# Kernel tuning notes

Hardware: AMD Instinct MI355X
Metric: run time of the kernel (lower is better)

Reference implementation:

```python
import jax, jax.numpy as jnp
import numpy as np

HEADS = 4
LOCAL_CTX = 8  # local_attn_ctx (stride)


def _strided_transpose(x, n_ctx, local_ctx):
    # [B, n_ctx, E] -> reshape [B, n_ctx//local, local, E] -> swap -> [B, n_ctx, E]
    B, _, E = x.shape
    bT = n_ctx // local_ctx
    return x.reshape(B, bT, local_ctx, E).transpose(0, 2, 1, 3).reshape(B, n_ctx, E)


def _strided_untranspose(a, n_ctx, local_ctx):
    B, _, E = a.shape
    bT = n_ctx // local_ctx
    return a.reshape(B, local_ctx, bT, E).transpose(0, 2, 1, 3).reshape(B, n_ctx, E)


def setup_inputs() -> dict:
    key = jax.random.key(0)
    ks = jax.random.split(key, 6)
    B, T, E = 2048, 64, 256
    value = jax.random.normal(ks[0], (B, T, E), dtype=jnp.float32)
    k_in = jax.random.normal(ks[1], (B, T, E), dtype=jnp.float32)
    query = jax.random.normal(ks[2], (B, T, E), dtype=jnp.float32)
    mask = jnp.ones((B, T), dtype=jnp.int32)  # unused by the block
    W_ff = jax.random.normal(ks[3], (256, T * E), dtype=jnp.float32) * (1.0 / np.sqrt(T * E))
    b_ff = jax.random.normal(ks[4], (256,), dtype=jnp.float32) * 0.01
    return {"value": value, "key": k_in, "query": query, "mask": mask, "W_ff": W_ff, "b_ff": b_ff}


def reference(value, key, query, mask, W_ff, b_ff):
    B, n_ctx, E = query.shape
    # strided transpose of q, k, v
    q = _strided_transpose(query, n_ctx, LOCAL_CTX)
    k = _strided_transpose(key, n_ctx, LOCAL_CTX)
    v = _strided_transpose(value, n_ctx, LOCAL_CTX)
    scale = 1.0 / np.sqrt(E // HEADS)  # n_state = embd // heads
    w = jax.nn.softmax(jnp.einsum('bqe,bke->bqk', q, k) * scale, axis=-1)
    a = jnp.einsum('bqk,bke->bqe', w, v)
    attention = _strided_untranspose(a, n_ctx, LOCAL_CTX)
    # residual + dropout (eval-mode identity)
    x = attention + query
    # flatten-linear + ReLU
    out = jax.nn.relu(x.reshape(B, n_ctx * E) @ W_ff.T + b_ff)
    return (out, attention)
```

## Files before the change

### kernel.cpp

```cpp
#include <hip/hip_runtime.h>
#include <stdint.h>

typedef __attribute__((ext_vector_type(8))) short s16x8;
typedef __attribute__((ext_vector_type(4))) float f32x4;

__device__ __forceinline__ unsigned short f2bf(float f) {
  unsigned int u = __float_as_uint(f);
  u += 0x7fffu + ((u >> 16) & 1u);
  return (unsigned short)(u >> 16);
}
__device__ __forceinline__ float bf2f(unsigned short h) {
  return __uint_as_float(((unsigned int)h) << 16);
}
__device__ __forceinline__ f32x4 mfma16(s16x8 a, s16x8 b, f32x4 c) {
  return __builtin_amdgcn_mfma_f32_16x16x32_bf16(a, b, c, 0, 0, 0);
}

#define KH_STR 136
#define VT_STR 72
#define P_STR  72

__global__ __launch_bounds__(256) void attn_kernel(
    const float* __restrict__ Vg, const float* __restrict__ Kg,
    const float* __restrict__ Qg, float* __restrict__ attn_out,
    unsigned short* __restrict__ xb ) {
  __shared__ __align__(16) char smem[46080];
  unsigned short* KhL = (unsigned short*)smem;
  unsigned short* KlL = (unsigned short*)(smem + 17408);
  unsigned short* VtL = (unsigned short*)smem;
  unsigned short* PL  = (unsigned short*)(smem + 36864);

  const int b = blockIdx.x;
  const int tid = threadIdx.x;
  const int lane = tid & 63;
  const int w = tid >> 6;
  const int n = lane & 15;
  const int q = lane >> 4;

  const float* Qb = Qg + (size_t)b * 64 * 256;
  const float* Kb = Kg + (size_t)b * 64 * 256;
  const float* Vb = Vg + (size_t)b * 64 * 256;

  f32x4 accS[4];
#pragma unroll
  for (int c = 0; c < 4; ++c) accS[c] = f32x4{0.f, 0.f, 0.f, 0.f};

  for (int ph = 0; ph < 2; ++ph) {
    const int e0 = ph * 128;
#pragma unroll
    for (int it = 0; it < 8; ++it) {
      int i = it * 256 + tid;
      int row = i >> 5;
      int c4 = i & 31;
      float4 v = *(const float4*)(Kb + row * 256 + e0 + c4 * 4);
      ushort4 hi, lo;
      hi.x = f2bf(v.x); lo.x = f2bf(v.x - bf2f(hi.x));
      hi.y = f2bf(v.y); lo.y = f2bf(v.y - bf2f(hi.y));
      hi.z = f2bf(v.z); lo.z = f2bf(v.z - bf2f(hi.z));
      hi.w = f2bf(v.w); lo.w = f2bf(v.w - bf2f(hi.w));
      *(ushort4*)(KhL + row * KH_STR + c4 * 4) = hi;
      *(ushort4*)(KlL + row * KH_STR + c4 * 4) = lo;
    }
    __syncthreads();
#pragma unroll
    for (int kk = 0; kk < 4; ++kk) {
      const float* qsrc = Qb + (16 * w + n) * 256 + e0 + kk * 32 + q * 8;
      float4 a0 = *(const float4*)qsrc;
      float4 a1 = *(const float4*)(qsrc + 4);
      float av[8] = {a0.x, a0.y, a0.z, a0.w, a1.x, a1.y, a1.z, a1.w};
      s16x8 qh, ql;
#pragma unroll
      for (int j = 0; j < 8; ++j) {
        unsigned short h = f2bf(av[j]);
        qh[j] = (short)h;
        ql[j] = (short)f2bf(av[j] - bf2f(h));
      }
      const int colb = kk * 32 + q * 8;
#pragma unroll
      for (int c = 0; c < 4; ++c) {
        s16x8 kh = *(const s16x8*)(KhL + (16 * c + n) * KH_STR + colb);
        s16x8 kl = *(const s16x8*)(KlL + (16 * c + n) * KH_STR + colb);
        accS[c] = mfma16(qh, kh, accS[c]);
        accS[c] = mfma16(qh, kl, accS[c]);
        accS[c] = mfma16(ql, kh, accS[c]);
      }
    }
    __syncthreads();
  }

  const float scale = 0.125f;
  float p[4][4];
#pragma unroll
  for (int r = 0; r < 4; ++r) {
    float m = -1e30f;
#pragma unroll
    for (int c = 0; c < 4; ++c) m = fmaxf(m, accS[c][r]);
#pragma unroll
    for (int mk = 1; mk < 16; mk <<= 1) m = fmaxf(m, __shfl_xor(m, mk, 64));
    float s = 0.f;
#pragma unroll
    for (int c = 0; c < 4; ++c) {
      float e = __expf((accS[c][r] - m) * scale);
      p[c][r] = e;
      s += e;
    }
#pragma unroll
    for (int mk = 1; mk < 16; mk <<= 1) s += __shfl_xor(s, mk, 64);
    float inv = 1.0f / s;
#pragma unroll
    for (int c = 0; c < 4; ++c) p[c][r] *= inv;
  }

#pragma unroll 4
  for (int t2 = 0; t2 < 32; ++t2) {
    int t = t2 * 2;
    float v0 = Vb[t * 256 + tid];
    float v1 = Vb[(t + 1) * 256 + tid];
    unsigned int pk = (unsigned int)f2bf(v0) | ((unsigned int)f2bf(v1) << 16);
    *(unsigned int*)(VtL + tid * VT_STR + t) = pk;
  }
#pragma unroll
  for (int r = 0; r < 4; ++r) {
    int row = 16 * w + 4 * q + r;
#pragma unroll
    for (int c = 0; c < 4; ++c) PL[row * P_STR + 16 * c + n] = f2bf(p[c][r]);
  }
  __syncthreads();

  f32x4 accA[16];
#pragma unroll
  for (int c = 0; c < 16; ++c) accA[c] = f32x4{0.f, 0.f, 0.f, 0.f};
#pragma unroll
  for (int ks = 0; ks < 2; ++ks) {
    const int colb = ks * 32 + q * 8;
    s16x8 af = *(const s16x8*)(PL + (16 * w + n) * P_STR + colb);
#pragma unroll
    for (int c = 0; c < 16; ++c) {
      s16x8 bf = *(const s16x8*)(VtL + (16 * c + n) * VT_STR + colb);
      accA[c] = mfma16(af, bf, accA[c]);
    }
  }

#pragma unroll
  for (int r = 0; r < 4; ++r) {
    int t = 16 * w + 4 * q + r;
    size_t base = ((size_t)b * 64 + t) * 256;
#pragma unroll
    for (int c = 0; c < 16; ++c) {
      int e = 16 * c + n;
      float aval = accA[c][r];
      attn_out[base + e] = aval;
      if (xb) xb[base + e] = f2bf(aval + Qb[t * 256 + e]);
    }
  }
}

__global__ __launch_bounds__(256) void w2b_kernel(const float* __restrict__ W,
                                                  unsigned short* __restrict__ Wb) {
  int i = blockIdx.x * 256 + threadIdx.x;
  float4 v = ((const float4*)W)[i];
  ushort4 o;
  o.x = f2bf(v.x); o.y = f2bf(v.y); o.z = f2bf(v.z); o.w = f2bf(v.w);
  ((ushort4*)Wb)[i] = o;
}

template <bool USE_XB>
__global__ __launch_bounds__(256) void ff_kernel(
    const unsigned short* __restrict__ xb, const float* __restrict__ attn,
    const float* __restrict__ query, const unsigned short* __restrict__ Wb,
    float* __restrict__ part, int kchunk) {
  __shared__ __align__(16) unsigned short As[64 * 72];
  __shared__ __align__(16) unsigned short Bs[64 * 72];
  const int tid = threadIdx.x;
  const int lane = tid & 63, w = tid >> 6, n = lane & 15, q = lane >> 4;
  const int m0 = blockIdx.x * 64;
  const int n0 = blockIdx.y * 64;
  const int k0 = blockIdx.z * kchunk;

  f32x4 acc[4];
#pragma unroll
  for (int c = 0; c < 4; ++c) acc[c] = f32x4{0.f, 0.f, 0.f, 0.f};

  const int srow = tid >> 3;
  const int scol = (tid & 7) * 8;

  for (int kk = 0; kk < kchunk; kk += 64) {
#pragma unroll
    for (int rr = 0; rr < 2; ++rr) {
      int row = rr * 32 + srow;
      size_t ga = (size_t)(m0 + row) * 16384 + k0 + kk + scol;
      if (USE_XB) {
        *(uint4*)(As + row * 72 + scol) = *(const uint4*)(xb + ga);
      } else {
        float4 a0 = *(const float4*)(attn + ga);
        float4 a1 = *(const float4*)(attn + ga + 4);
        float4 q0 = *(const float4*)(query + ga);
        float4 q1 = *(const float4*)(query + ga + 4);
        ushort4 h0, h1;
        h0.x = f2bf(a0.x + q0.x); h0.y = f2bf(a0.y + q0.y);
        h0.z = f2bf(a0.z + q0.z); h0.w = f2bf(a0.w + q0.w);
        h1.x = f2bf(a1.x + q1.x); h1.y = f2bf(a1.y + q1.y);
        h1.z = f2bf(a1.z + q1.z); h1.w = f2bf(a1.w + q1.w);
        *(ushort4*)(As + row * 72 + scol) = h0;
        *(ushort4*)(As + row * 72 + scol + 4) = h1;
      }
      size_t gw = (size_t)(n0 + row) * 16384 + k0 + kk + scol;
      *(uint4*)(Bs + row * 72 + scol) = *(const uint4*)(Wb + gw);
    }
    __syncthreads();
#pragma unroll
    for (int ks = 0; ks < 2; ++ks) {
      const int colb = ks * 32 + q * 8;
      s16x8 af = *(const s16x8*)(As + (16 * w + n) * 72 + colb);
#pragma unroll
      for (int c = 0; c < 4; ++c) {
        s16x8 bf = *(const s16x8*)(Bs + (16 * c + n) * 72 + colb);
        acc[c] = mfma16(af, bf, acc[c]);
      }
    }
    __syncthreads();
  }
#pragma unroll
  for (int r = 0; r < 4; ++r) {
    int m = m0 + 16 * w + 4 * q + r;
#pragma unroll
    for (int c = 0; c < 4; ++c) {
      int nn = n0 + 16 * c + n;
      part[((size_t)blockIdx.z * 2048 + m) * 256 + nn] = acc[c][r];
    }
  }
}

__global__ __launch_bounds__(256) void relu_kernel(const float* __restrict__ part,
                                                   const float* __restrict__ bias,
                                                   float* __restrict__ out, int KS) {
  int idx = blockIdx.x * 256 + threadIdx.x;
  float s = bias[idx & 255];
  for (int ks = 0; ks < KS; ++ks) s += part[(size_t)ks * 2048 * 256 + idx];
  out[idx] = fmaxf(s, 0.f);
}

extern "C" void kernel_launch(void* const* d_in, const int* in_sizes, int n_in,
                              void* d_out, int out_size, void* d_ws, size_t ws_size,
                              hipStream_t stream) {
  const float* value = (const float*)d_in[0];
  const float* key   = (const float*)d_in[1];
  const float* query = (const float*)d_in[2];
  const float* W_ff  = (const float*)d_in[4];
  const float* b_ff  = (const float*)d_in[5];

  float* out  = (float*)d_out;
  float* attn = out + (size_t)2048 * 256;

  const int KS = 4;
  const size_t wb_bytes   = (size_t)256 * 16384 * 2;
  const size_t part_bytes = (size_t)KS * 2048 * 256 * 4;
  const size_t xb_bytes   = (size_t)2048 * 64 * 256 * 2;
  unsigned short* Wb = (unsigned short*)d_ws;
  float* part = (float*)((char*)d_ws + wb_bytes);
  bool use_xb = ws_size >= wb_bytes + part_bytes + xb_bytes;
  unsigned short* xb =
      use_xb ? (unsigned short*)((char*)d_ws + wb_bytes + part_bytes) : nullptr;

  w2b_kernel<<<4096, 256, 0, stream>>>(W_ff, Wb);
  attn_kernel<<<2048, 256, 0, stream>>>(value, key, query, attn, xb);
  dim3 gb(32, 4, KS);
  if (use_xb)
    ff_kernel<true><<<gb, 256, 0, stream>>>(xb, nullptr, nullptr, Wb, part, 16384 / KS);
  else
    ff_kernel<false><<<gb, 256, 0, stream>>>(nullptr, attn, query, Wb, part, 16384 / KS);
  relu_kernel<<<2048, 256, 0, stream>>>(part, b_ff, out, KS);
}
```

Measured before the change: 287.4 us.

## Shrink LDS, prefetch V into registers, swizzle K tiles, stage coalesced output

```diff
diff --git a/kernel.cpp b/kernel.cpp
--- a/kernel.cpp
+++ b/kernel.cpp
@@ -16,19 +16,15 @@
   return __builtin_amdgcn_mfma_f32_16x16x32_bf16(a, b, c, 0, 0, 0);
 }
 
-#define KH_STR 136
-#define VT_STR 72
-#define P_STR  72
-
 __global__ __launch_bounds__(256) void attn_kernel(
     const float* __restrict__ Vg, const float* __restrict__ Kg,
     const float* __restrict__ Qg, float* __restrict__ attn_out,
     unsigned short* __restrict__ xb ) {
-  __shared__ __align__(16) char smem[46080];
-  unsigned short* KhL = (unsigned short*)smem;
-  unsigned short* KlL = (unsigned short*)(smem + 17408);
+  __shared__ __align__(16) char smem[32768];
+  char* KhB = smem;
+  char* KlB = smem + 16384;
   unsigned short* VtL = (unsigned short*)smem;
-  unsigned short* PL  = (unsigned short*)(smem + 36864);
+  unsigned short* PL = (unsigned short*)(smem + 18432);
 
   const int b = blockIdx.x;
   const int tid = threadIdx.x;
@@ -44,6 +40,8 @@
   f32x4 accS[4];
 #pragma unroll
   for (int c = 0; c < 4; ++c) accS[c] = f32x4{0.f, 0.f, 0.f, 0.f};
+
+  float va[16], vbv[16];
 
   for (int ph = 0; ph < 2; ++ph) {
     const int e0 = ph * 128;
@@ -58,16 +56,31 @@
       hi.y = f2bf(v.y); lo.y = f2bf(v.y - bf2f(hi.y));
       hi.z = f2bf(v.z); lo.z = f2bf(v.z - bf2f(hi.z));
       hi.w = f2bf(v.w); lo.w = f2bf(v.w - bf2f(hi.w));
-      *(ushort4*)(KhL + row * KH_STR + c4 * 4) = hi;
-      *(ushort4*)(KlL + row * KH_STR + c4 * 4) = lo;
+      int off = row * 256 + ((c4 * 8) ^ ((row & 7) << 4));
+      *(ushort4*)(KhB + off) = hi;
+      *(ushort4*)(KlB + off) = lo;
     }
     __syncthreads();
+    float4 qf0[4], qf1[4];
 #pragma unroll
     for (int kk = 0; kk < 4; ++kk) {
       const float* qsrc = Qb + (16 * w + n) * 256 + e0 + kk * 32 + q * 8;
-      float4 a0 = *(const float4*)qsrc;
-      float4 a1 = *(const float4*)(qsrc + 4);
-      float av[8] = {a0.x, a0.y, a0.z, a0.w, a1.x, a1.y, a1.z, a1.w};
+      qf0[kk] = *(const float4*)qsrc;
+      qf1[kk] = *(const float4*)(qsrc + 4);
+    }
+    if (ph == 1) {
+#pragma unroll
+      for (int i = 0; i < 16; ++i) {
+        int j = i * 256 + tid, e = j & 127, tp = j >> 7;
+        va[i] = Vb[(2 * tp) * 256 + e];
+        vbv[i] = Vb[(2 * tp + 1) * 256 + e];
+      }
+    }
+    __builtin_amdgcn_s_setprio(1);
+#pragma unroll
+    for (int kk = 0; kk < 4; ++kk) {
+      float av[8] = {qf0[kk].x, qf0[kk].y, qf0[kk].z, qf0[kk].w,
+                     qf1[kk].x, qf1[kk].y, qf1[kk].z, qf1[kk].w};
       s16x8 qh, ql;
 #pragma unroll
       for (int j = 0; j < 8; ++j) {
@@ -75,16 +88,19 @@
         qh[j] = (short)h;
         ql[j] = (short)f2bf(av[j] - bf2f(h));
       }
-      const int colb = kk * 32 + q * 8;
+      const int cb = (kk * 32 + q * 8) * 2;
 #pragma unroll
       for (int c = 0; c < 4; ++c) {
-        s16x8 kh = *(const s16x8*)(KhL + (16 * c + n) * KH_STR + colb);
-        s16x8 kl = *(const s16x8*)(KlL + (16 * c + n) * KH_STR + colb);
+        int row = 16 * c + n;
+        int off = row * 256 + (cb ^ ((row & 7) << 4));
+        s16x8 kh = *(const s16x8*)(KhB + off);
+        s16x8 kl = *(const s16x8*)(KlB + off);
         accS[c] = mfma16(qh, kh, accS[c]);
         accS[c] = mfma16(qh, kl, accS[c]);
         accS[c] = mfma16(ql, kh, accS[c]);
       }
     }
+    __builtin_amdgcn_s_setprio(0);
     __syncthreads();
   }
 
@@ -111,46 +127,104 @@
     for (int c = 0; c < 4; ++c) p[c][r] *= inv;
   }
 
-#pragma unroll 4
-  for (int t2 = 0; t2 < 32; ++t2) {
-    int t = t2 * 2;
-    float v0 = Vb[t * 256 + tid];
-    float v1 = Vb[(t + 1) * 256 + tid];
-    unsigned int pk = (unsigned int)f2bf(v0) | ((unsigned int)f2bf(v1) << 16);
-    *(unsigned int*)(VtL + tid * VT_STR + t) = pk;
+#pragma unroll
+  for (int i = 0; i < 16; ++i) {
+    int j = i * 256 + tid, e = j & 127, tp = j >> 7;
+    unsigned int pk = (unsigned int)f2bf(va[i]) | ((unsigned int)f2bf(vbv[i]) << 16);
+    *(unsigned int*)(VtL + e * 72 + 2 * tp) = pk;
   }
 #pragma unroll
   for (int r = 0; r < 4; ++r) {
     int row = 16 * w + 4 * q + r;
 #pragma unroll
-    for (int c = 0; c < 4; ++c) PL[row * P_STR + 16 * c + n] = f2bf(p[c][r]);
+    for (int c = 0; c < 4; ++c) PL[row * 72 + 16 * c + n] = f2bf(p[c][r]);
+  }
+#pragma unroll
+  for (int i = 0; i < 16; ++i) {
+    int j = i * 256 + tid, e = j & 127, tp = j >> 7;
+    va[i] = Vb[(2 * tp) * 256 + 128 + e];
+    vbv[i] = Vb[(2 * tp + 1) * 256 + 128 + e];
   }
   __syncthreads();
 
   f32x4 accA[16];
 #pragma unroll
   for (int c = 0; c < 16; ++c) accA[c] = f32x4{0.f, 0.f, 0.f, 0.f};
+
+  __builtin_amdgcn_s_setprio(1);
 #pragma unroll
   for (int ks = 0; ks < 2; ++ks) {
     const int colb = ks * 32 + q * 8;
-    s16x8 af = *(const s16x8*)(PL + (16 * w + n) * P_STR + colb);
-#pragma unroll
-    for (int c = 0; c < 16; ++c) {
-      s16x8 bf = *(const s16x8*)(VtL + (16 * c + n) * VT_STR + colb);
+    s16x8 af = *(const s16x8*)(PL + (16 * w + n) * 72 + colb);
+#pragma unroll
+    for (int c = 0; c < 8; ++c) {
+      s16x8 bf = *(const s16x8*)(VtL + (16 * c + n) * 72 + colb);
       accA[c] = mfma16(af, bf, accA[c]);
     }
   }
-
-#pragma unroll
-  for (int r = 0; r < 4; ++r) {
-    int t = 16 * w + 4 * q + r;
-    size_t base = ((size_t)b * 64 + t) * 256;
-#pragma unroll
-    for (int c = 0; c < 16; ++c) {
-      int e = 16 * c + n;
-      float aval = accA[c][r];
-      attn_out[base + e] = aval;
-      if (xb) xb[base + e] = f2bf(aval + Qb[t * 256 + e]);
+  __builtin_amdgcn_s_setprio(0);
+  __syncthreads();
+#pragma unroll
+  for (int i = 0; i < 16; ++i) {
+    int j = i * 256 + tid, e = j & 127, tp = j >> 7;
+    unsigned int pk = (unsigned int)f2bf(va[i]) | ((unsigned int)f2bf(vbv[i]) << 16);
+    *(unsigned int*)(VtL + e * 72 + 2 * tp) = pk;
+  }
+  __syncthreads();
+  __builtin_amdgcn_s_setprio(1);
+#pragma unroll
+  for (int ks = 0; ks < 2; ++ks) {
+    const int colb = ks * 32 + q * 8;
+    s16x8 af = *(const s16x8*)(PL + (16 * w + n) * 72 + colb);
+#pragma unroll
+    for (int c = 8; c < 16; ++c) {
+      s16x8 bf = *(const s16x8*)(VtL + (16 * (c - 8) + n) * 72 + colb);
+      accA[c] = mfma16(af, bf, accA[c]);
+    }
+  }
+  __builtin_amdgcn_s_setprio(0);
+
+  if (xb) {
+#pragma unroll
+    for (int h = 0; h < 2; ++h) {
+      __syncthreads();
+#pragma unroll
+      for (int r = 0; r < 4; ++r) {
+        int t = 16 * w + 4 * q + r;
+        int sw = (t & 7) << 4;
+#pragma unroll
+        for (int c8 = 0; c8 < 8; ++c8) {
+          int c = h * 8 + c8;
+          int el = 16 * c8 + n;
+          *(float*)(smem + t * 512 + ((el * 4) ^ sw)) = accA[c][r];
+        }
+      }
+      __syncthreads();
+#pragma unroll
+      for (int i = 0; i < 8; ++i) {
+        int f4 = i * 256 + tid;
+        int row = f4 >> 5;
+        int col4 = f4 & 31;
+        int e = h * 128 + col4 * 4;
+        float4 av = *(const float4*)(smem + row * 512 + ((col4 * 16) ^ ((row & 7) << 4)));
+        float4 qv = *(const float4*)(Qb + row * 256 + e);
+        size_t base = ((size_t)b * 64 + row) * 256 + e;
+        *(float4*)(attn_out + base) = av;
+        ushort4 o;
+        o.x = f2bf(av.x + qv.x);
+        o.y = f2bf(av.y + qv.y);
+        o.z = f2bf(av.z + qv.z);
+        o.w = f2bf(av.w + qv.w);
+        *(ushort4*)(xb + base) = o;
+      }
+    }
+  } else {
+#pragma unroll
+    for (int r = 0; r < 4; ++r) {
+      int t = 16 * w + 4 * q + r;
+      size_t base = ((size_t)b * 64 + t) * 256;
+#pragma unroll
+      for (int c = 0; c < 16; ++c) attn_out[base + 16 * c + n] = accA[c][r];
     }
   }
 }
```

Measured after the change: 262.5 us. -8.7%, faster.
